# Kernel tuning notes

Measured on AMD Instinct MI355X. Metric: run time of the kernel, lower is better.

Reference implementation:

```python
import jax, jax.numpy as jnp
import numpy as np

NUM_RBF = 16
RBF_D_MIN, RBF_D_MAX = 2.0, 22.0
CB_A, CB_B, CB_C = -0.58273431, 0.56802827, -0.54067466
TOP_K = 32
MAX_REL = 32
NPOS = 16
HID = 128
LN_EPS = 1e-5


def _gather_nodes(nodes, idx):
    # nodes: (B, L, D), idx: (B, L, K) -> (B, L, K, D)
    return jax.vmap(lambda n, i: n[i])(nodes, idx)


def _rbf_encode(D):
    mu = jnp.linspace(RBF_D_MIN, RBF_D_MAX, NUM_RBF, dtype=D.dtype)
    sigma = (RBF_D_MAX - RBF_D_MIN) / NUM_RBF
    return jnp.exp(-((D[..., None] - mu) ** 2) / (sigma ** 2))


def setup_inputs() -> dict:
    key = jax.random.key(0)
    ks = jax.random.split(key, 4)
    B, L = 2, 2048
    X = jax.random.normal(ks[0], (B, L, 4, 3), jnp.float32) * 10.0
    residue_mask = jnp.ones((B, L), jnp.float32)
    R_idx = jnp.arange(B * L, dtype=jnp.int32).reshape(B, L)
    chain_labels = jnp.zeros((B, L), jnp.int32)
    # learned params
    W_pos = jax.random.normal(ks[1], (NPOS, 2 * MAX_REL + 2), jnp.float32) * 0.05
    b_pos = jnp.zeros((NPOS,), jnp.float32)
    W_edge = jax.random.normal(ks[2], (HID, 25 * NUM_RBF + NPOS), jnp.float32) * 0.02
    ln_gamma = jnp.ones((HID,), jnp.float32)
    ln_beta = jnp.zeros((HID,), jnp.float32)
    return {"X": X, "residue_mask": residue_mask, "R_idx": R_idx,
            "chain_labels": chain_labels, "W_pos": W_pos, "b_pos": b_pos,
            "W_edge": W_edge, "ln_gamma": ln_gamma, "ln_beta": ln_beta}


def reference(X, residue_mask, R_idx, chain_labels, W_pos, b_pos, W_edge, ln_gamma, ln_beta):
    B, L = X.shape[0], X.shape[1]
    K = min(TOP_K, L)
    # virtual CB from backbone N, CA, C
    N, CA, C = X[..., 0, :], X[..., 1, :], X[..., 2, :]
    b = CA - N
    c = C - CA
    a = jnp.cross(b, c, axis=-1)
    CB = (CB_A * a + CB_B * b + CB_C * c + CA)[..., None, :]
    atoms_5 = jnp.concatenate([X, CB], axis=-2)  # (B, L, 5, 3)
    # kNN on CA coords with invalid residues pushed far away
    diff = CA[:, :, None, :] - CA[:, None, :, :]
    dist_sq = jnp.sum(diff * diff, axis=-1)  # (B, L, L)
    inv_mask = 1.0 - residue_mask
    dist_sq = dist_sq + inv_mask[:, None, :] * 1e6
    _, E_idx = jax.lax.top_k(-dist_sq, K)  # smallest-k indices, (B, L, K)
    # gather neighbor 5-atom coords and compute 25 pairwise distances
    Xf = atoms_5.reshape(B, L, 15)
    Xg = _gather_nodes(Xf, E_idx).reshape(B, L, K, 5, 3)
    d2 = jnp.sum((atoms_5[:, :, None, :, None, :] - Xg[:, :, :, None, :, :]) ** 2, axis=-1)
    D = jnp.sqrt(d2 + 1e-6)  # (B, L, K, 5, 5)
    rbf = _rbf_encode(D).reshape(B, L, K, 25 * NUM_RBF)
    # positional encodings (standard ProteinMPNN form)
    Rg = _gather_nodes(R_idx[..., None], E_idx)[..., 0]  # (B, L, K)
    Cg = _gather_nodes(chain_labels[..., None], E_idx)[..., 0]
    d_rel = Rg - R_idx[:, :, None]
    same_chain = (Cg == chain_labels[:, :, None])
    d_clip = jnp.clip(d_rel + MAX_REL, 0, 2 * MAX_REL)
    d_final = jnp.where(same_chain, d_clip, 2 * MAX_REL + 1)
    oh = jax.nn.one_hot(d_final, 2 * MAX_REL + 2, dtype=rbf.dtype)
    pos_enc = jnp.einsum('blkc,pc->blkp', oh, W_pos) + b_pos
    # edge embedding + layernorm
    edge_input = jnp.concatenate([pos_enc, rbf], axis=-1)  # (B, L, K, 416)
    h = jnp.einsum('blkf,hf->blkh', edge_input, W_edge)
    mean = jnp.mean(h, axis=-1, keepdims=True)
    var = jnp.var(h, axis=-1, keepdims=True)
    E = (h - mean) * jax.lax.rsqrt(var + LN_EPS) * ln_gamma + ln_beta
    return E_idx, E
```

## Files before the change

### kernel.cpp

```cpp
#include <hip/hip_runtime.h>
#include <hip/hip_bf16.h>

#define LEN   2048
#define KNB   32
#define HID   128
#define FS    520

typedef unsigned long long ull;
typedef unsigned int uint32;
typedef float f32x4  __attribute__((ext_vector_type(4)));
typedef float f32x16 __attribute__((ext_vector_type(16)));

__device__ __forceinline__ void bar_lgkm() {
    asm volatile("s_waitcnt lgkmcnt(0)" ::: "memory");
    __builtin_amdgcn_s_barrier();
    asm volatile("" ::: "memory");
}

__global__ __launch_bounds__(256) void topk_kernel(
    const float* __restrict__ X, const float* __restrict__ mask,
    const float* __restrict__ W_edge, int* __restrict__ Wf8,
    float* __restrict__ eidx_out) {
    const int bid = blockIdx.x;
    const int tid = threadIdx.x;

    if (bid >= 2 * LEN) {
        const int t = (bid - 2 * LEN) * 256 + tid;
        if (t < 13312) {
            const float4 w = ((const float4*)W_edge)[t];
            int r = __builtin_amdgcn_cvt_pk_fp8_f32(w.x, w.y, 0, false);
            r = __builtin_amdgcn_cvt_pk_fp8_f32(w.z, w.w, r, true);
            Wf8[t] = r;
        }
        return;
    }

    const int row = bid;
    const int b = row >> 11;
    const int i = row & (LEN - 1);

    __shared__ int hist[512];
    __shared__ ull cand[LEN];
    __shared__ int candcnt;
    __shared__ int selB;

    const float* Xb = X + (size_t)b * LEN * 12;
    const float* mb = mask + (size_t)b * LEN;
    const float cax = Xb[i * 12 + 3];
    const float cay = Xb[i * 12 + 4];
    const float caz = Xb[i * 12 + 5];

    uint32 d2b[8];
#pragma unroll
    for (int q = 0; q < 8; ++q) {
        const int j = q * 256 + tid;
        float dx = __fsub_rn(cax, Xb[j * 12 + 3]);
        float dy = __fsub_rn(cay, Xb[j * 12 + 4]);
        float dz = __fsub_rn(caz, Xb[j * 12 + 5]);
        float d2 = __fadd_rn(__fadd_rn(__fmul_rn(dx, dx), __fmul_rn(dy, dy)),
                             __fmul_rn(dz, dz));
        d2 = __fadd_rn(d2, __fmul_rn(__fsub_rn(1.0f, mb[j]), 1000000.0f));
        d2b[q] = __float_as_uint(d2);
    }

    hist[tid] = 0; hist[tid + 256] = 0;
    if (tid == 0) candcnt = 0;
    __syncthreads();
#pragma unroll
    for (int q = 0; q < 8; ++q) atomicAdd(&hist[d2b[q] >> 22], 1);
    __syncthreads();

    if (tid < 64) {
        int loc[8];
        int s = 0;
#pragma unroll
        for (int t = 0; t < 8; ++t) { loc[t] = hist[tid * 8 + t]; s += loc[t]; }
        int incl = s;
#pragma unroll
        for (int off = 1; off < 64; off <<= 1) {
            int o = __shfl_up(incl, off, 64);
            if (tid >= off) incl += o;
        }
        const int excl = incl - s;
        if (excl < KNB && incl >= KNB) {
            int c = excl;
#pragma unroll
            for (int t = 0; t < 8; ++t) {
                int c2 = c + loc[t];
                if (c < KNB && c2 >= KNB) selB = tid * 8 + t;
                c = c2;
            }
        }
    }
    __syncthreads();
    const uint32 B = (uint32)selB;

#pragma unroll
    for (int q = 0; q < 8; ++q) {
        if ((d2b[q] >> 22) <= B) {
            int p = atomicAdd(&candcnt, 1);
            cand[p] = (((ull)d2b[q]) << 32) | (uint32)(q * 256 + tid);
        }
    }
    __syncthreads();
    const int M = candcnt;

    for (int c = tid; c < M; c += 256) {
        const ull k = cand[c];
        int r = 0;
        for (int m = 0; m < M; ++m) r += (cand[m] < k);
        if (r < KNB)
            eidx_out[(size_t)row * KNB + r] = (float)(uint32)(k & 0xFFFFFFFFull);
    }
}

__device__ __forceinline__ void load_res_atoms(const float* __restrict__ p, float* dst) {
    const float Nx = p[0], Ny = p[1], Nz = p[2];
    const float Ax = p[3], Ay = p[4], Az = p[5];
    const float Cx = p[6], Cy = p[7], Cz = p[8];
    const float Ox = p[9], Oy = p[10], Oz = p[11];
    const float bx = Ax - Nx, by = Ay - Ny, bz = Az - Nz;
    const float cx = Cx - Ax, cy = Cy - Ay, cz = Cz - Az;
    const float axv = by * cz - bz * cy;
    const float ayv = bz * cx - bx * cz;
    const float azv = bx * cy - by * cx;
    dst[0] = Nx;  dst[1] = Ny;  dst[2] = Nz;
    dst[3] = Ax;  dst[4] = Ay;  dst[5] = Az;
    dst[6] = Cx;  dst[7] = Cy;  dst[8] = Cz;
    dst[9] = Ox;  dst[10] = Oy; dst[11] = Oz;
    dst[12] = -0.58273431f * axv + 0.56802827f * bx + -0.54067466f * cx + Ax;
    dst[13] = -0.58273431f * ayv + 0.56802827f * by + -0.54067466f * cy + Ay;
    dst[14] = -0.58273431f * azv + 0.56802827f * bz + -0.54067466f * cz + Az;
}

__device__ __forceinline__ int pk4(float a, float b, float c, float d) {
    int r = __builtin_amdgcn_cvt_pk_fp8_f32(a, b, 0, false);
    return __builtin_amdgcn_cvt_pk_fp8_f32(c, d, r, true);
}

#define E1  3.2053337e-1f
#define E3  3.2931300e-2f
#define E5  3.3834001e-3f
#define E7  3.4760500e-4f

__device__ __forceinline__ void compute_features(
    int tid, int Ri, int Ci,
    const float* __restrict__ wposL,
    const int* jR, const int* jC,
    const float (*natoms)[15], const float* iatoms,
    unsigned char* featF8) {
    {
        const int e = tid >> 4, p = tid & 15;
        const int drel = jR[e] - Ri;
        const int same = (jC[e] == Ci);
        int dc = drel + 32;
        dc = dc < 0 ? 0 : (dc > 64 ? 64 : dc);
        const int df = same ? dc : 65;
        const float v = wposL[p * 66 + df];
        const int pb = __builtin_amdgcn_cvt_pk_fp8_f32(v, 0.0f, 0, false);
        featF8[e * FS + p] = (unsigned char)(pb & 0xFF);
    }
#pragma unroll
    for (int it = 0; it < 2; ++it) {
        const int task = tid + it * 512;
        if (task < 800) {
            const int mn = task >> 5, e = task & 31;
            const int m = mn / 5, n = mn - m * 5;
            const float ax = iatoms[m * 3 + 0];
            const float ay = iatoms[m * 3 + 1];
            const float az = iatoms[m * 3 + 2];
            const float* na = &natoms[e][n * 3];
            const float dx = ax - na[0], dy = ay - na[1], dz = az - na[2];
            const float D = sqrtf(dx * dx + dy * dy + dz * dz + 1e-6f);
            const float Dc = fminf(D, 40.0f);
            const float v4 = Dc - 7.3333333f;
            const float A4  = __expf(-0.64f * v4 * v4);
            const float C4  = __expf(1.7066667f * v4);
            const float Ci4 = 1.0f / C4;
            ull lo, hi2;
            {
                const float f3 = A4 * Ci4 * E1;
                const float f2 = f3 * Ci4 * E3;
                const float f1 = f2 * Ci4 * E5;
                const float f0 = f1 * Ci4 * E7;
                const float f5 = A4 * C4 * E1;
                const float f6 = f5 * C4 * E3;
                const float f7 = f6 * C4 * E5;
                lo = (uint32)pk4(f0, f1, f2, f3)
                   | ((ull)(uint32)pk4(A4, f5, f6, f7) << 32);
            }
            const float v12 = Dc - 18.0f;
            const float A12  = __expf(-0.64f * v12 * v12);
            const float C12  = C4 * 1.24140e-8f;
            const float Ci12 = Ci4 * 8.05543e7f;
            {
                const float f11 = A12 * Ci12 * E1;
                const float f10 = f11 * Ci12 * E3;
                const float f9  = f10 * Ci12 * E5;
                const float f8  = f9  * Ci12 * E7;
                const float f13 = A12 * C12 * E1;
                const float f14 = f13 * C12 * E3;
                const float f15 = f14 * C12 * E5;
                hi2 = (uint32)pk4(f8, f9, f10, f11)
                    | ((ull)(uint32)pk4(A12, f13, f14, f15) << 32);
            }
            *(ull*)(featF8 + e * FS + 16 + mn * 16)     = lo;
            *(ull*)(featF8 + e * FS + 16 + mn * 16 + 8) = hi2;
        }
    }
}

__global__ __launch_bounds__(512, 4) void edge_kernel(
    const float* __restrict__ X,
    const int* __restrict__ Ridx, const int* __restrict__ Chain,
    const float* __restrict__ W_pos, const float* __restrict__ b_pos,
    const unsigned char* __restrict__ Wf8,
    const float* __restrict__ lng, const float* __restrict__ lnb,
    const float* __restrict__ eidx_f, float* __restrict__ outE) {
    const int tid = threadIdx.x;
    const int row0 = blockIdx.x * 8;
    const int b = row0 >> 11;
    const int i0 = row0 & (LEN - 1);

    __shared__ __align__(16) unsigned char featF8[2][32 * FS];
    __shared__ float natoms[8][32][15];
    __shared__ float iatoms[8][16];
    __shared__ float wposL[16 * 66];
    __shared__ __align__(16) float pS[2][32][4], pQ[2][32][4];
    __shared__ float gbuf[HID], bbuf[HID];
    __shared__ int jR[8][KNB], jC[8][KNB];
    __shared__ int riS[8], ciS[8];

    const float* Xb = X + (size_t)b * LEN * 12;

    const int w = tid >> 6, l = tid & 63;
    const int rowsel = w >> 2, cg = w & 3;
    const int e32 = l & 31, hi = l >> 5;

    long wreg[26];
    {
        const unsigned char* wb = Wf8 + (size_t)(cg * 32 + e32) * 416 + hi * 8;
#pragma unroll
        for (int ks = 0; ks < 26; ++ks)
            wreg[ks] = *(const long*)(wb + ks * 16);
    }

    for (int t = tid; t < 1056; t += 512)
        wposL[t] = W_pos[t] + b_pos[t / 66];
    if (tid < 256) {
        const int r = tid >> 5, e = tid & 31;
        const int j = (int)eidx_f[(size_t)(row0 + r) * KNB + e];
        jR[r][e] = Ridx[b * LEN + j];
        jC[r][e] = Chain[b * LEN + j];
        load_res_atoms(Xb + j * 12, &natoms[r][e][0]);
    } else if (tid < 264) {
        const int r = tid - 256;
        load_res_atoms(Xb + (size_t)(i0 + r) * 12, &iatoms[r][0]);
    } else if (tid < 272) {
        riS[tid - 264] = Ridx[b * LEN + i0 + (tid - 264)];
    } else if (tid < 280) {
        ciS[tid - 272] = Chain[b * LEN + i0 + (tid - 272)];
    } else if (tid >= 384) {
        const int t2 = tid - 384;
        gbuf[t2] = lng[t2];
        bbuf[t2] = lnb[t2];
    }
    bar_lgkm();

    compute_features(tid, riS[0], ciS[0], wposL, jR[0], jC[0],
                     natoms[0], iatoms[0], featF8[0]);
    compute_features(tid, riS[1], ciS[1], wposL, jR[1], jC[1],
                     natoms[1], iatoms[1], featF8[1]);
    bar_lgkm();

    for (int it = 0; it < 4; ++it) {
        const int myrow = row0 + 2 * it + rowsel;

        f32x16 acc = {0.f, 0.f, 0.f, 0.f, 0.f, 0.f, 0.f, 0.f,
                      0.f, 0.f, 0.f, 0.f, 0.f, 0.f, 0.f, 0.f};
        {
            const unsigned char* fb = featF8[rowsel] + e32 * FS + hi * 8;
#pragma unroll
            for (int ks = 0; ks < 26; ++ks) {
                const long a = *(const long*)(fb + ks * 16);
                acc = __builtin_amdgcn_mfma_f32_32x32x16_fp8_fp8(wreg[ks], a, acc, 0, 0, 0);
            }
        }
        {
            float s = 0.f, q = 0.f;
#pragma unroll
            for (int r = 0; r < 16; ++r) { s += acc[r]; q += acc[r] * acc[r]; }
            s += __shfl_xor(s, 32, 64);
            q += __shfl_xor(q, 32, 64);
            if (hi == 0) {
                pS[rowsel][e32][cg] = s;
                pQ[rowsel][e32][cg] = q;
            }
        }
        bar_lgkm();

        {
            const float4 ps = *(const float4*)&pS[rowsel][e32][0];
            const float4 pq = *(const float4*)&pQ[rowsel][e32][0];
            const float s = ps.x + ps.y + ps.z + ps.w;
            const float q = pq.x + pq.y + pq.z + pq.w;
            const float mean = s * (1.0f / 128.0f);
            const float rstd = rsqrtf(q * (1.0f / 128.0f) - mean * mean + 1e-5f);
            const int cb = cg * 32 + hi * 4;
            float* orow = outE + ((size_t)myrow * KNB + e32) * HID + cb;
#pragma unroll
            for (int j = 0; j < 4; ++j) {
                const float4 gg = *(const float4*)&gbuf[cb + 8 * j];
                const float4 bb = *(const float4*)&bbuf[cb + 8 * j];
                float4 o;
                o.x = (acc[4 * j + 0] - mean) * rstd * gg.x + bb.x;
                o.y = (acc[4 * j + 1] - mean) * rstd * gg.y + bb.y;
                o.z = (acc[4 * j + 2] - mean) * rstd * gg.z + bb.z;
                o.w = (acc[4 * j + 3] - mean) * rstd * gg.w + bb.w;
                *(float4*)(orow + 8 * j) = o;
            }
        }
        if (it < 3) {
            const int na = 2 * it + 2, nb = 2 * it + 3;
            compute_features(tid, riS[na], ciS[na], wposL, jR[na], jC[na],
                             natoms[na], iatoms[na], featF8[0]);
            compute_features(tid, riS[nb], ciS[nb], wposL, jR[nb], jC[nb],
                             natoms[nb], iatoms[nb], featF8[1]);
        }
        bar_lgkm();
    }
}

extern "C" void kernel_launch(void* const* d_in, const int* in_sizes, int n_in,
                              void* d_out, int out_size, void* d_ws, size_t ws_size,
                              hipStream_t stream) {
    const float* X      = (const float*)d_in[0];
    const float* mask   = (const float*)d_in[1];
    const int*   Ridx   = (const int*)d_in[2];
    const int*   Chain  = (const int*)d_in[3];
    const float* W_pos  = (const float*)d_in[4];
    const float* b_pos  = (const float*)d_in[5];
    const float* W_edge = (const float*)d_in[6];
    const float* lng    = (const float*)d_in[7];
    const float* lnb    = (const float*)d_in[8];

    float* out  = (float*)d_out;
    float* eidx = out;
    float* E    = out + (size_t)2 * LEN * KNB;

    unsigned char* Wf8 = (unsigned char*)d_ws;

    const int nrow = 2 * LEN;
    topk_kernel<<<nrow + 52, 256, 0, stream>>>(X, mask, W_edge, (int*)Wf8, eidx);
    edge_kernel<<<nrow / 8, 512, 0, stream>>>(X, Ridx, Chain, W_pos, b_pos, Wf8,
                                              lng, lnb, eidx, E);
}
```

Measured before the change: 54.70 us.

## Quad-buffer edge features to overlap next-row feature build with MFMA GEMM

```diff
diff --git a/kernel.cpp b/kernel.cpp
--- a/kernel.cpp
+++ b/kernel.cpp
@@ -4,7 +4,8 @@
 #define LEN   2048
 #define KNB   32
 #define HID   128
-#define FS    520
+#define FS    440
+#define FBSZ  (32 * FS)
 
 typedef unsigned long long ull;
 typedef unsigned int uint32;
@@ -145,7 +146,7 @@
 
 __device__ __forceinline__ void compute_features(
     int tid, int Ri, int Ci,
-    const float* __restrict__ wposL,
+    const __bf16* __restrict__ wposL,
     const int* jR, const int* jC,
     const float (*natoms)[15], const float* iatoms,
     unsigned char* featF8) {
@@ -156,7 +157,7 @@
         int dc = drel + 32;
         dc = dc < 0 ? 0 : (dc > 64 ? 64 : dc);
         const int df = same ? dc : 65;
-        const float v = wposL[p * 66 + df];
+        const float v = (float)wposL[p * 66 + df];
         const int pb = __builtin_amdgcn_cvt_pk_fp8_f32(v, 0.0f, 0, false);
         featF8[e * FS + p] = (unsigned char)(pb & 0xFF);
     }
@@ -210,6 +211,53 @@
     }
 }
 
+__device__ __forceinline__ f32x16 gemm26(const unsigned char* fb, const long* wreg) {
+    f32x16 acc = {0.f, 0.f, 0.f, 0.f, 0.f, 0.f, 0.f, 0.f,
+                  0.f, 0.f, 0.f, 0.f, 0.f, 0.f, 0.f, 0.f};
+#pragma unroll
+    for (int ks = 0; ks < 26; ++ks) {
+        const long a = *(const long*)(fb + ks * 16);
+        acc = __builtin_amdgcn_mfma_f32_32x32x16_fp8_fp8(wreg[ks], a, acc, 0, 0, 0);
+    }
+    return acc;
+}
+
+__device__ __forceinline__ void partials(
+    const f32x16& acc, float (*pSb)[4], float (*pQb)[4],
+    int e32, int cg, int hi) {
+    float s = 0.f, q = 0.f;
+#pragma unroll
+    for (int r = 0; r < 16; ++r) { s += acc[r]; q += acc[r] * acc[r]; }
+    s += __shfl_xor(s, 32, 64);
+    q += __shfl_xor(q, 32, 64);
+    if (hi == 0) { pSb[e32][cg] = s; pQb[e32][cg] = q; }
+}
+
+__device__ __forceinline__ void ln_store(
+    const f32x16& acc, const float (*pSb)[4], const float (*pQb)[4],
+    int e32, int cg, int hi, int myrow,
+    const float* gbuf, const float* bbuf, float* __restrict__ outE) {
+    const float4 ps = *(const float4*)&pSb[e32][0];
+    const float4 pq = *(const float4*)&pQb[e32][0];
+    const float s = ps.x + ps.y + ps.z + ps.w;
+    const float q = pq.x + pq.y + pq.z + pq.w;
+    const float mean = s * (1.0f / 128.0f);
+    const float rstd = rsqrtf(q * (1.0f / 128.0f) - mean * mean + 1e-5f);
+    const int cb = cg * 32 + hi * 4;
+    float* orow = outE + ((size_t)myrow * KNB + e32) * HID + cb;
+#pragma unroll
+    for (int j = 0; j < 4; ++j) {
+        const float4 gg = *(const float4*)&gbuf[cb + 8 * j];
+        const float4 bb = *(const float4*)&bbuf[cb + 8 * j];
+        float4 o;
+        o.x = (acc[4 * j + 0] - mean) * rstd * gg.x + bb.x;
+        o.y = (acc[4 * j + 1] - mean) * rstd * gg.y + bb.y;
+        o.z = (acc[4 * j + 2] - mean) * rstd * gg.z + bb.z;
+        o.w = (acc[4 * j + 3] - mean) * rstd * gg.w + bb.w;
+        *(float4*)(orow + 8 * j) = o;
+    }
+}
+
 __global__ __launch_bounds__(512, 4) void edge_kernel(
     const float* __restrict__ X,
     const int* __restrict__ Ridx, const int* __restrict__ Chain,
@@ -222,11 +270,12 @@
     const int b = row0 >> 11;
     const int i0 = row0 & (LEN - 1);
 
-    __shared__ __align__(16) unsigned char featF8[2][32 * FS];
+    __shared__ __align__(16) unsigned char featF8[4 * FBSZ];
     __shared__ float natoms[8][32][15];
     __shared__ float iatoms[8][16];
-    __shared__ float wposL[16 * 66];
-    __shared__ __align__(16) float pS[2][32][4], pQ[2][32][4];
+    __shared__ __bf16 wposL[16 * 66];
+    __shared__ __align__(16) float pS[2][2][32][4];
+    __shared__ __align__(16) float pQ[2][2][32][4];
     __shared__ float gbuf[HID], bbuf[HID];
     __shared__ int jR[8][KNB], jC[8][KNB];
     __shared__ int riS[8], ciS[8];
@@ -246,7 +295,7 @@
     }
 
     for (int t = tid; t < 1056; t += 512)
-        wposL[t] = W_pos[t] + b_pos[t / 66];
+        wposL[t] = (__bf16)(W_pos[t] + b_pos[t / 66]);
     if (tid < 256) {
         const int r = tid >> 5, e = tid & 31;
         const int j = (int)eidx_f[(size_t)(row0 + r) * KNB + e];
@@ -268,67 +317,52 @@
     bar_lgkm();
 
     compute_features(tid, riS[0], ciS[0], wposL, jR[0], jC[0],
-                     natoms[0], iatoms[0], featF8[0]);
+                     natoms[0], iatoms[0], featF8 + 0 * FBSZ);
     compute_features(tid, riS[1], ciS[1], wposL, jR[1], jC[1],
-                     natoms[1], iatoms[1], featF8[1]);
-    bar_lgkm();
-
-    for (int it = 0; it < 4; ++it) {
-        const int myrow = row0 + 2 * it + rowsel;
-
-        f32x16 acc = {0.f, 0.f, 0.f, 0.f, 0.f, 0.f, 0.f, 0.f,
-                      0.f, 0.f, 0.f, 0.f, 0.f, 0.f, 0.f, 0.f};
-        {
-            const unsigned char* fb = featF8[rowsel] + e32 * FS + hi * 8;
-#pragma unroll
-            for (int ks = 0; ks < 26; ++ks) {
-                const long a = *(const long*)(fb + ks * 16);
-                acc = __builtin_amdgcn_mfma_f32_32x32x16_fp8_fp8(wreg[ks], a, acc, 0, 0, 0);
-            }
-        }
-        {
-            float s = 0.f, q = 0.f;
-#pragma unroll
-            for (int r = 0; r < 16; ++r) { s += acc[r]; q += acc[r] * acc[r]; }
-            s += __shfl_xor(s, 32, 64);
-            q += __shfl_xor(q, 32, 64);
-            if (hi == 0) {
-                pS[rowsel][e32][cg] = s;
-                pQ[rowsel][e32][cg] = q;
-            }
-        }
-        bar_lgkm();
-
-        {
-            const float4 ps = *(const float4*)&pS[rowsel][e32][0];
-            const float4 pq = *(const float4*)&pQ[rowsel][e32][0];
-            const float s = ps.x + ps.y + ps.z + ps.w;
-            const float q = pq.x + pq.y + pq.z + pq.w;
-            const float mean = s * (1.0f / 128.0f);
-            const float rstd = rsqrtf(q * (1.0f / 128.0f) - mean * mean + 1e-5f);
-            const int cb = cg * 32 + hi * 4;
-            float* orow = outE + ((size_t)myrow * KNB + e32) * HID + cb;
-#pragma unroll
-            for (int j = 0; j < 4; ++j) {
-                const float4 gg = *(const float4*)&gbuf[cb + 8 * j];
-                const float4 bb = *(const float4*)&bbuf[cb + 8 * j];
-                float4 o;
-                o.x = (acc[4 * j + 0] - mean) * rstd * gg.x + bb.x;
-                o.y = (acc[4 * j + 1] - mean) * rstd * gg.y + bb.y;
-                o.z = (acc[4 * j + 2] - mean) * rstd * gg.z + bb.z;
-                o.w = (acc[4 * j + 3] - mean) * rstd * gg.w + bb.w;
-                *(float4*)(orow + 8 * j) = o;
-            }
-        }
-        if (it < 3) {
-            const int na = 2 * it + 2, nb = 2 * it + 3;
-            compute_features(tid, riS[na], ciS[na], wposL, jR[na], jC[na],
-                             natoms[na], iatoms[na], featF8[0]);
-            compute_features(tid, riS[nb], ciS[nb], wposL, jR[nb], jC[nb],
-                             natoms[nb], iatoms[nb], featF8[1]);
-        }
-        bar_lgkm();
-    }
+                     natoms[1], iatoms[1], featF8 + 1 * FBSZ);
+    bar_lgkm();
+
+    const unsigned char* fbMine01 = featF8 + rowsel * FBSZ + e32 * FS + hi * 8;
+    const unsigned char* fbMine23 = featF8 + ((2 + rowsel) & 3) * FBSZ + e32 * FS + hi * 8;
+
+    f32x16 accA, accB;
+
+    accA = gemm26(fbMine01, wreg);
+    compute_features(tid, riS[2], ciS[2], wposL, jR[2], jC[2],
+                     natoms[2], iatoms[2], featF8 + 2 * FBSZ);
+    compute_features(tid, riS[3], ciS[3], wposL, jR[3], jC[3],
+                     natoms[3], iatoms[3], featF8 + 3 * FBSZ);
+    partials(accA, pS[0][rowsel], pQ[0][rowsel], e32, cg, hi);
+    bar_lgkm();
+
+    ln_store(accA, pS[0][rowsel], pQ[0][rowsel], e32, cg, hi,
+             row0 + 0 + rowsel, gbuf, bbuf, outE);
+    accB = gemm26(fbMine23, wreg);
+    compute_features(tid, riS[4], ciS[4], wposL, jR[4], jC[4],
+                     natoms[4], iatoms[4], featF8 + 0 * FBSZ);
+    compute_features(tid, riS[5], ciS[5], wposL, jR[5], jC[5],
+                     natoms[5], iatoms[5], featF8 + 1 * FBSZ);
+    partials(accB, pS[1][rowsel], pQ[1][rowsel], e32, cg, hi);
+    bar_lgkm();
+
+    ln_store(accB, pS[1][rowsel], pQ[1][rowsel], e32, cg, hi,
+             row0 + 2 + rowsel, gbuf, bbuf, outE);
+    accA = gemm26(fbMine01, wreg);
+    compute_features(tid, riS[6], ciS[6], wposL, jR[6], jC[6],
+                     natoms[6], iatoms[6], featF8 + 2 * FBSZ);
+    compute_features(tid, riS[7], ciS[7], wposL, jR[7], jC[7],
+                     natoms[7], iatoms[7], featF8 + 3 * FBSZ);
+    partials(accA, pS[0][rowsel], pQ[0][rowsel], e32, cg, hi);
+    bar_lgkm();
+
+    ln_store(accA, pS[0][rowsel], pQ[0][rowsel], e32, cg, hi,
+             row0 + 4 + rowsel, gbuf, bbuf, outE);
+    accB = gemm26(fbMine23, wreg);
+    partials(accB, pS[1][rowsel], pQ[1][rowsel], e32, cg, hi);
+    bar_lgkm();
+
+    ln_store(accB, pS[1][rowsel], pQ[1][rowsel], e32, cg, hi,
+             row0 + 6 + rowsel, gbuf, bbuf, outE);
 }
 
 extern "C" void kernel_launch(void* const* d_in, const int* in_sizes, int n_in,
```

Measured after the change: 56.10 us. 2.6% more time.
